# Optimization experiments

Hardware: AMD Instinct MI355X
Metric: run time of the kernel (lower is better)

## Reference

```python
import jax, jax.numpy as jnp
import numpy as np

# Static diagonal offsets of the SparseDIA matrix (eqx static field).
OFFSETS = (-128, -64, -8, -1, 0, 1, 8, 64, 128)
N = 8192   # matrix dimension (diags.shape[1])
M = 4096   # number of dense columns in `other`


def setup_inputs() -> dict:
    key = jax.random.key(0)
    k1, k2 = jax.random.split(key)
    diags = jax.random.normal(k1, (len(OFFSETS), N), dtype=jnp.float32)
    other = jax.random.normal(k2, (N, M), dtype=jnp.float32)
    return {"diags": diags, "other": other}


def reference(diags, other):
    """SparseDIA._matmul_dense(left_matmul=True): out = A_dia @ other.

    For each static offset k, rows [top:bottom] of the output accumulate
    diag[start:end] (the valid part of the stored diagonal) times the
    matching rows of `other`. Offsets are Python ints, so all slices are
    static and jit-compatible.
    """
    n = other.shape[0]
    out = jnp.zeros_like(other)
    for k, offset in enumerate(OFFSETS):
        start = max(0, offset)
        end = min(n, n + offset)
        top = max(0, -offset)
        bottom = top + (end - start)
        out = out.at[top:bottom, :].add(
            diags[k, start:end, None] * other[start:end, :]
        )
    return out
```

## Files before the change

### kernel.cpp

```cpp
#include <hip/hip_runtime.h>


#define DIA_N 8192
#define DIA_M 4096
#define M4 (DIA_M / 4)

__global__ __launch_bounds__(256) void sparse_dia_kernel(
    const float* __restrict__ diags,
    const float* __restrict__ other,
    float* __restrict__ out)
{
    constexpr int OFF[9] = {-128, -64, -8, -1, 0, 1, 8, 64, 128};

    const int r  = blockIdx.y;
    const int c4 = blockIdx.x * blockDim.x + threadIdx.x;

    const float4* __restrict__ o4 = (const float4*)other;
    float4* __restrict__ out4     = (float4*)out;

    float4 acc = make_float4(0.f, 0.f, 0.f, 0.f);

    if (r >= 128 && r < DIA_N - 128) {
#pragma unroll
        for (int k = 0; k < 9; ++k) {
            const int q = r + OFF[k];
            const float d = diags[k * DIA_N + q];
            const float4 v = o4[q * M4 + c4];
            acc.x += d * v.x;
            acc.y += d * v.y;
            acc.z += d * v.z;
            acc.w += d * v.w;
        }
    } else {
#pragma unroll
        for (int k = 0; k < 9; ++k) {
            const int q = r + OFF[k];
            if (q >= 0 && q < DIA_N) {
                const float d = diags[k * DIA_N + q];
                const float4 v = o4[q * M4 + c4];
                acc.x += d * v.x;
                acc.y += d * v.y;
                acc.z += d * v.z;
                acc.w += d * v.w;
            }
        }
    }

    out4[r * M4 + c4] = acc;
}

extern "C" void kernel_launch(void* const* d_in, const int* in_sizes, int n_in,
                              void* d_out, int out_size, void* d_ws, size_t ws_size,
                              hipStream_t stream) {
    const float* diags = (const float*)d_in[0];
    const float* other = (const float*)d_in[1];
    float* out         = (float*)d_out;

    dim3 block(256, 1, 1);
    dim3 grid(M4 / 256, DIA_N, 1);
    sparse_dia_kernel<<<grid, block, 0, stream>>>(diags, other, out);
}
```

Baseline: 268.9 us.

## Tile output rows and stage a haloed slab of other in LDS

Each block now computes a 256-row by 8-float4-column tile. It first loads the 512-row haloed slab of `other` (zero-padded at the matrix edges) into shared memory, so the nine diagonal reads reuse on-chip data instead of re-reading rows from global memory or L2. The far diagonals (offsets 0, ±64, ±128) are read from a register copy of strided LDS rows. The near diagonals (±1, ±8) are read directly from LDS. The cost is a 2x halo read amplification per tile, a 64KB LDS footprint that limits occupancy to two blocks per CU, and a synchronisation before compute.

```diff
diff --git a/kernel.cpp b/kernel.cpp
--- a/kernel.cpp
+++ b/kernel.cpp
@@ -1,52 +1,99 @@
 #include <hip/hip_runtime.h>
 
 
-#define DIA_N 8192
-#define DIA_M 4096
-#define M4 (DIA_M / 4)
+#define DIA_N   8192
+#define M4      1024
+#define TC      8
+#define TR      256
+#define LROWS   (TR + 256)
+#define NSTRIPE (M4 / TC)
+#define NTILE   (DIA_N / TR)
 
-__global__ __launch_bounds__(256) void sparse_dia_kernel(
+__global__ __launch_bounds__(256, 2) void sparse_dia_kernel(
     const float* __restrict__ diags,
     const float* __restrict__ other,
     float* __restrict__ out)
 {
-    constexpr int OFF[9] = {-128, -64, -8, -1, 0, 1, 8, 64, 128};
+    __shared__ float4 lds[LROWS * TC];
 
-    const int r  = blockIdx.y;
-    const int c4 = blockIdx.x * blockDim.x + threadIdx.x;
+    const int b  = blockIdx.x;
+    const int s  = b & (NSTRIPE - 1);
+    const int i  = b >> 7;
+    const int r0 = i * TR;
+    const int c0 = s * TC;
 
     const float4* __restrict__ o4 = (const float4*)other;
     float4* __restrict__ out4     = (float4*)out;
+    const int t = threadIdx.x;
 
-    float4 acc = make_float4(0.f, 0.f, 0.f, 0.f);
+#pragma unroll
+    for (int u = 0; u < 16; ++u) {
+        const int idx = t + 256 * u;
+        const int lr  = idx >> 3;
+        const int c   = idx & 7;
+        const int q   = r0 - 128 + lr;
+        float4 v = make_float4(0.f, 0.f, 0.f, 0.f);
+        if (q >= 0 && q < DIA_N) v = o4[q * M4 + c0 + c];
+        lds[idx] = v;
+    }
+    __syncthreads();
 
-    if (r >= 128 && r < DIA_N - 128) {
+    const int c  = t & 7;
+    const int rg = t >> 3;
+
+    float4 acc[8];
 #pragma unroll
-        for (int k = 0; k < 9; ++k) {
-            const int q = r + OFF[k];
-            const float d = diags[k * DIA_N + q];
-            const float4 v = o4[q * M4 + c4];
-            acc.x += d * v.x;
-            acc.y += d * v.y;
-            acc.z += d * v.z;
-            acc.w += d * v.w;
-        }
-    } else {
+    for (int j = 0; j < 8; ++j) acc[j] = make_float4(0.f, 0.f, 0.f, 0.f);
+
+    float4 w[16];
 #pragma unroll
-        for (int k = 0; k < 9; ++k) {
-            const int q = r + OFF[k];
-            if (q >= 0 && q < DIA_N) {
-                const float d = diags[k * DIA_N + q];
-                const float4 v = o4[q * M4 + c4];
-                acc.x += d * v.x;
-                acc.y += d * v.y;
-                acc.z += d * v.z;
-                acc.w += d * v.w;
-            }
+    for (int m = 0; m < 16; ++m) w[m] = lds[(rg + 32 * m) * TC + c];
+
+    constexpr int FAR_OFF[5] = {-128, -64, 0, 64, 128};
+    constexpr int FAR_K[5]   = {0, 1, 4, 7, 8};
+#pragma unroll
+    for (int f = 0; f < 5; ++f) {
+        const int off = FAR_OFF[f];
+        const int e4  = off / 32 + 4;
+#pragma unroll
+        for (int j = 0; j < 8; ++j) {
+            const int r = r0 + rg + 32 * j;
+            int q = r + off;
+            q = max(0, min(DIA_N - 1, q));
+            const float d  = diags[FAR_K[f] * DIA_N + q];
+            const float4 v = w[j + e4];
+            acc[j].x += d * v.x;
+            acc[j].y += d * v.y;
+            acc[j].z += d * v.z;
+            acc[j].w += d * v.w;
         }
     }
 
-    out4[r * M4 + c4] = acc;
+    constexpr int NEAR_OFF[4] = {-8, -1, 1, 8};
+    constexpr int NEAR_K[4]   = {2, 3, 5, 6};
+#pragma unroll
+    for (int f = 0; f < 4; ++f) {
+        const int off = NEAR_OFF[f];
+#pragma unroll
+        for (int j = 0; j < 8; ++j) {
+            const int lrow = rg + 32 * j;
+            const int r = r0 + lrow;
+            int q = r + off;
+            q = max(0, min(DIA_N - 1, q));
+            const float d  = diags[NEAR_K[f] * DIA_N + q];
+            const float4 v = lds[(lrow + 128 + off) * TC + c];
+            acc[j].x += d * v.x;
+            acc[j].y += d * v.y;
+            acc[j].z += d * v.z;
+            acc[j].w += d * v.w;
+        }
+    }
+
+#pragma unroll
+    for (int j = 0; j < 8; ++j) {
+        const int r = r0 + rg + 32 * j;
+        out4[r * M4 + c0 + c] = acc[j];
+    }
 }
 
 extern "C" void kernel_launch(void* const* d_in, const int* in_sizes, int n_in,
@@ -57,6 +104,6 @@
     float* out         = (float*)d_out;
 
     dim3 block(256, 1, 1);
-    dim3 grid(M4 / 256, DIA_N, 1);
+    dim3 grid(NSTRIPE * NTILE, 1, 1);
     sparse_dia_kernel<<<grid, block, 0, stream>>>(diags, other, out);
 }
```

Measured after the change: 272.6 us. No clear change (+1.4%).
